# Optimization experiments

Hardware: AMD Instinct MI355X
Metric: run time of the kernel (lower is better)

The kernel has to match this reference:

```python
import jax, jax.numpy as jnp
import numpy as np


def setup_inputs() -> dict:
    key = jax.random.key(0)
    k1, k2 = jax.random.split(key)
    B, N, M, D = 16, 2048, 2048, 3
    predictions = jax.random.normal(k1, (B, N, D), dtype=jnp.float32)
    targets = jax.random.normal(k2, (B, M, D), dtype=jnp.float32)
    return {"predictions": predictions, "targets": targets}


def reference(predictions, targets):
    # Batched pairwise squared distances: [B, N, M]
    # d(i,j) = |x_i|^2 + |y_j|^2 - 2 x_i . y_j
    xx = jnp.sum(predictions * predictions, axis=-1)  # [B, N]
    yy = jnp.sum(targets * targets, axis=-1)          # [B, M]
    xy = jnp.einsum("bnd,bmd->bnm", predictions, targets)  # [B, N, M]
    P = xx[:, :, None] + yy[:, None, :] - 2.0 * xy    # [B, N, M]
    # Chamfer: sum of per-point nearest-neighbor squared distances, both directions
    loss = jnp.sum(jnp.min(P, axis=2)) + jnp.sum(jnp.min(P, axis=1))
    return loss
```

## Files before the change

### kernel.cpp

```cpp
#include <hip/hip_runtime.h>
#include <math.h>


typedef float v2f __attribute__((ext_vector_type(2)));

#define NPTS    2048
#define NCOMBO  32
#define KSLICE  32
#define SLICE   64
#define SPT     16
#define NBLK2   256

__device__ __forceinline__ v2f pkfma(v2f a, v2f b, v2f c) {
#if __has_builtin(__builtin_elementwise_fma)
    return __builtin_elementwise_fma(a, b, c);
#else
    v2f d; d.x = fmaf(a.x, b.x, c.x); d.y = fmaf(a.y, b.y, c.y); return d;
#endif
}

__global__ __launch_bounds__(256, 2) void chamfer_partial(
    const float* __restrict__ preds,
    const float* __restrict__ tgts,
    float* __restrict__ partial,
    int* __restrict__ counter)
{
    __shared__ __align__(16) float qx[2][SLICE];
    __shared__ __align__(16) float qy[2][SLICE];
    __shared__ __align__(16) float qz[2][SLICE];
    __shared__ __align__(16) float qw[2][SLICE];

    const int bid   = blockIdx.x;
    const int combo = bid & (NCOMBO - 1);
    const int spair = bid >> 5;
    const int dir   = combo >> 4;
    const int b     = combo & 15;

    const int sb    = threadIdx.x >> 7;
    const int tt    = threadIdx.x & 127;
    const int slice = spair * 2 + sb;

    if (bid == 0 && threadIdx.x == 0) *counter = 0;

    const float* src = (dir ? tgts : preds) + (size_t)b * NPTS * 3;
    const float* opp = (dir ? preds : tgts) + (size_t)b * NPTS * 3;

    if (tt < SLICE) {
        const int jj = slice * SLICE + tt;
        const float y0 = opp[3 * jj + 0];
        const float y1 = opp[3 * jj + 1];
        const float y2 = opp[3 * jj + 2];
        qx[sb][tt] = y0;
        qy[sb][tt] = y1;
        qz[sb][tt] = y2;
        qw[sb][tt] = y0 * y0 + y1 * y1 + y2 * y2;
    }

    v2f nn0[SPT], nn1[SPT], nn2[SPT];
    float m[SPT];
    #pragma unroll
    for (int k = 0; k < SPT; k++) {
        const int i = tt + 128 * k;
        const float a0 = -2.0f * src[3 * i + 0];
        const float a1 = -2.0f * src[3 * i + 1];
        const float a2 = -2.0f * src[3 * i + 2];
        nn0[k] = (v2f){a0, a0};
        nn1[k] = (v2f){a1, a1};
        nn2[k] = (v2f){a2, a2};
        m[k]   = INFINITY;
    }
    __syncthreads();

    #pragma unroll 2
    for (int jg = 0; jg < SLICE / 4; jg++) {
        const float4 X = *(const float4*)&qx[sb][4 * jg];
        const float4 Y = *(const float4*)&qy[sb][4 * jg];
        const float4 Z = *(const float4*)&qz[sb][4 * jg];
        const float4 W = *(const float4*)&qw[sb][4 * jg];
        const v2f Xa = {X.x, X.y}, Xb = {X.z, X.w};
        const v2f Ya = {Y.x, Y.y}, Yb = {Y.z, Y.w};
        const v2f Za = {Z.x, Z.y}, Zb = {Z.z, Z.w};
        const v2f Wa = {W.x, W.y}, Wb = {W.z, W.w};
        #pragma unroll
        for (int k = 0; k < SPT; k++) {
            const v2f sa = pkfma(nn0[k], Xa, pkfma(nn1[k], Ya, pkfma(nn2[k], Za, Wa)));
            m[k] = fminf(fminf(m[k], sa.x), sa.y);
            const v2f sb2 = pkfma(nn0[k], Xb, pkfma(nn1[k], Yb, pkfma(nn2[k], Zb, Wb)));
            m[k] = fminf(fminf(m[k], sb2.x), sb2.y);
        }
    }

    float* pp = partial + ((size_t)combo * KSLICE + slice) * NPTS;
    #pragma unroll
    for (int k = 0; k < SPT; k++)
        pp[tt + 128 * k] = m[k];
}

__global__ __launch_bounds__(256) void chamfer_reduce(
    const float* __restrict__ preds,
    const float* __restrict__ tgts,
    const float* __restrict__ partial,
    float* __restrict__ blocksum,
    int* __restrict__ counter,
    float* __restrict__ out)
{
    __shared__ float wsum[4];
    __shared__ bool  amLast;

    const int idx   = blockIdx.x * 256 + threadIdx.x;
    const int combo = idx >> 11;
    const int i     = idx & (NPTS - 1);
    const int dir   = combo >> 4;
    const int b     = combo & 15;

    const float* src = (dir ? tgts : preds) + (size_t)b * NPTS * 3;
    const float x0 = src[3 * i + 0];
    const float x1 = src[3 * i + 1];
    const float x2 = src[3 * i + 2];
    const float xx = x0 * x0 + x1 * x1 + x2 * x2;

    const float* pp = partial + (size_t)combo * KSLICE * NPTS + i;
    float mn = pp[0];
    #pragma unroll
    for (int s = 1; s < KSLICE; s++)
        mn = fminf(mn, pp[(size_t)s * NPTS]);

    float val = xx + mn;

    #pragma unroll
    for (int off = 32; off > 0; off >>= 1)
        val += __shfl_down(val, off, 64);

    const int lane = threadIdx.x & 63;
    const int wid  = threadIdx.x >> 6;
    if (lane == 0) wsum[wid] = val;
    __syncthreads();

    if (threadIdx.x == 0) {
        const float bsum = wsum[0] + wsum[1] + wsum[2] + wsum[3];
        __hip_atomic_store(&blocksum[blockIdx.x], bsum,
                           __ATOMIC_RELAXED, __HIP_MEMORY_SCOPE_AGENT);
        __threadfence();
        amLast = (atomicAdd(counter, 1) == NBLK2 - 1);
    }
    __syncthreads();

    if (amLast) {
        __threadfence();
        float v = __hip_atomic_load(&blocksum[threadIdx.x],
                                    __ATOMIC_RELAXED, __HIP_MEMORY_SCOPE_AGENT);
        #pragma unroll
        for (int off = 32; off > 0; off >>= 1)
            v += __shfl_down(v, off, 64);
        if (lane == 0) wsum[wid] = v;
        __syncthreads();
        if (threadIdx.x == 0)
            out[0] = wsum[0] + wsum[1] + wsum[2] + wsum[3];
    }
}

extern "C" void kernel_launch(void* const* d_in, const int* in_sizes, int n_in,
                              void* d_out, int out_size, void* d_ws, size_t ws_size,
                              hipStream_t stream) {
    const float* preds = (const float*)d_in[0];
    const float* tgts  = (const float*)d_in[1];
    float* out      = (float*)d_out;
    float* partial  = (float*)d_ws;
    float* blocksum = partial + (size_t)NCOMBO * KSLICE * NPTS;
    int*   counter  = (int*)(blocksum + NBLK2);

    chamfer_partial<<<NCOMBO * (KSLICE / 2), 256, 0, stream>>>(preds, tgts, partial, counter);
    chamfer_reduce<<<NBLK2, 256, 0, stream>>>(preds, tgts, partial, blocksum, counter, out);
}
```

Before: 77.06 us.

## Fuse partial-min and reduction kernels via per-combo last-block atomics

Merges the two kernels into one. The last block to finish each (direction, batch) combo, detected with a per-combo atomic counter, reduces that combo's 32 slice minima using float4 loads and adds the squared norms. A global counter then picks the final block to sum the 32 combo sums. This removes the second kernel launch and its gap, but adds a memset launch and serializes each combo's reduction into a single block.

Result: slower. 102.1 us (+32.5%).

```diff
diff --git a/kernel.cpp b/kernel.cpp
--- a/kernel.cpp
+++ b/kernel.cpp
@@ -9,7 +9,6 @@
 #define KSLICE  32
 #define SLICE   64
 #define SPT     16
-#define NBLK2   256
 
 __device__ __forceinline__ v2f pkfma(v2f a, v2f b, v2f c) {
 #if __has_builtin(__builtin_elementwise_fma)
@@ -19,16 +18,26 @@
 #endif
 }
 
-__global__ __launch_bounds__(256, 2) void chamfer_partial(
+__device__ __forceinline__ float4 fmin4(float4 a, float4 b) {
+    return make_float4(fminf(a.x, b.x), fminf(a.y, b.y),
+                       fminf(a.z, b.z), fminf(a.w, b.w));
+}
+
+__global__ __launch_bounds__(256, 2) void chamfer_fused(
     const float* __restrict__ preds,
     const float* __restrict__ tgts,
     float* __restrict__ partial,
-    int* __restrict__ counter)
+    float* __restrict__ combosum,
+    int* __restrict__ ccount,
+    int* __restrict__ gcount,
+    float* __restrict__ out)
 {
     __shared__ __align__(16) float qx[2][SLICE];
     __shared__ __align__(16) float qy[2][SLICE];
     __shared__ __align__(16) float qz[2][SLICE];
     __shared__ __align__(16) float qw[2][SLICE];
+    __shared__ float wsum[4];
+    __shared__ bool  amLast, amLast2;
 
     const int bid   = blockIdx.x;
     const int combo = bid & (NCOMBO - 1);
@@ -39,8 +48,6 @@
     const int sb    = threadIdx.x >> 7;
     const int tt    = threadIdx.x & 127;
     const int slice = spair * 2 + sb;
-
-    if (bid == 0 && threadIdx.x == 0) *counter = 0;
 
     const float* src = (dir ? tgts : preds) + (size_t)b * NPTS * 3;
     const float* opp = (dir ? preds : tgts) + (size_t)b * NPTS * 3;
@@ -94,43 +101,46 @@
     #pragma unroll
     for (int k = 0; k < SPT; k++)
         pp[tt + 128 * k] = m[k];
-}
 
-__global__ __launch_bounds__(256) void chamfer_reduce(
-    const float* __restrict__ preds,
-    const float* __restrict__ tgts,
-    const float* __restrict__ partial,
-    float* __restrict__ blocksum,
-    int* __restrict__ counter,
-    float* __restrict__ out)
-{
-    __shared__ float wsum[4];
-    __shared__ bool  amLast;
+    __syncthreads();
+    if (threadIdx.x == 0) {
+        __threadfence();
+        const int old = __hip_atomic_fetch_add(&ccount[combo], 1,
+                            __ATOMIC_ACQ_REL, __HIP_MEMORY_SCOPE_AGENT);
+        amLast = (old == 15);
+    }
+    __syncthreads();
+    if (!amLast) return;
+    __threadfence();
 
-    const int idx   = blockIdx.x * 256 + threadIdx.x;
-    const int combo = idx >> 11;
-    const int i     = idx & (NPTS - 1);
-    const int dir   = combo >> 4;
-    const int b     = combo & 15;
-
-    const float* src = (dir ? tgts : preds) + (size_t)b * NPTS * 3;
-    const float x0 = src[3 * i + 0];
-    const float x1 = src[3 * i + 1];
-    const float x2 = src[3 * i + 2];
-    const float xx = x0 * x0 + x1 * x1 + x2 * x2;
-
-    const float* pp = partial + (size_t)combo * KSLICE * NPTS + i;
-    float mn = pp[0];
-    #pragma unroll
-    for (int s = 1; s < KSLICE; s++)
-        mn = fminf(mn, pp[(size_t)s * NPTS]);
-
-    float val = xx + mn;
+    const float* base = partial + (size_t)combo * KSLICE * NPTS;
+    const int t = threadIdx.x;
+    float4 mnA = make_float4(INFINITY, INFINITY, INFINITY, INFINITY);
+    float4 mnB = mnA;
+    #pragma unroll 4
+    for (int s = 0; s < KSLICE; s++) {
+        mnA = fmin4(mnA, *(const float4*)&base[(size_t)s * NPTS + 4 * t]);
+        mnB = fmin4(mnB, *(const float4*)&base[(size_t)s * NPTS + 1024 + 4 * t]);
+    }
+    const float4 rA0 = *(const float4*)&src[12 * t + 0];
+    const float4 rA1 = *(const float4*)&src[12 * t + 4];
+    const float4 rA2 = *(const float4*)&src[12 * t + 8];
+    const float4 rB0 = *(const float4*)&src[3072 + 12 * t + 0];
+    const float4 rB1 = *(const float4*)&src[3072 + 12 * t + 4];
+    const float4 rB2 = *(const float4*)&src[3072 + 12 * t + 8];
+    float val =
+        (fmaf(rA0.x, rA0.x, fmaf(rA0.y, rA0.y, rA0.z * rA0.z)) + mnA.x) +
+        (fmaf(rA0.w, rA0.w, fmaf(rA1.x, rA1.x, rA1.y * rA1.y)) + mnA.y) +
+        (fmaf(rA1.z, rA1.z, fmaf(rA1.w, rA1.w, rA2.x * rA2.x)) + mnA.z) +
+        (fmaf(rA2.y, rA2.y, fmaf(rA2.z, rA2.z, rA2.w * rA2.w)) + mnA.w) +
+        (fmaf(rB0.x, rB0.x, fmaf(rB0.y, rB0.y, rB0.z * rB0.z)) + mnB.x) +
+        (fmaf(rB0.w, rB0.w, fmaf(rB1.x, rB1.x, rB1.y * rB1.y)) + mnB.y) +
+        (fmaf(rB1.z, rB1.z, fmaf(rB1.w, rB1.w, rB2.x * rB2.x)) + mnB.z) +
+        (fmaf(rB2.y, rB2.y, fmaf(rB2.z, rB2.z, rB2.w * rB2.w)) + mnB.w);
 
     #pragma unroll
     for (int off = 32; off > 0; off >>= 1)
         val += __shfl_down(val, off, 64);
-
     const int lane = threadIdx.x & 63;
     const int wid  = threadIdx.x >> 6;
     if (lane == 0) wsum[wid] = val;
@@ -138,24 +148,26 @@
 
     if (threadIdx.x == 0) {
         const float bsum = wsum[0] + wsum[1] + wsum[2] + wsum[3];
-        __hip_atomic_store(&blocksum[blockIdx.x], bsum,
+        __hip_atomic_store(&combosum[combo], bsum,
                            __ATOMIC_RELAXED, __HIP_MEMORY_SCOPE_AGENT);
         __threadfence();
-        amLast = (atomicAdd(counter, 1) == NBLK2 - 1);
+        const int old = __hip_atomic_fetch_add(gcount, 1,
+                            __ATOMIC_ACQ_REL, __HIP_MEMORY_SCOPE_AGENT);
+        amLast2 = (old == NCOMBO - 1);
     }
     __syncthreads();
+    if (!amLast2) return;
+    __threadfence();
 
-    if (amLast) {
-        __threadfence();
-        float v = __hip_atomic_load(&blocksum[threadIdx.x],
-                                    __ATOMIC_RELAXED, __HIP_MEMORY_SCOPE_AGENT);
+    if (threadIdx.x < 64) {
+        float v = (threadIdx.x < NCOMBO)
+            ? __hip_atomic_load(&combosum[threadIdx.x],
+                                __ATOMIC_RELAXED, __HIP_MEMORY_SCOPE_AGENT)
+            : 0.0f;
         #pragma unroll
         for (int off = 32; off > 0; off >>= 1)
             v += __shfl_down(v, off, 64);
-        if (lane == 0) wsum[wid] = v;
-        __syncthreads();
-        if (threadIdx.x == 0)
-            out[0] = wsum[0] + wsum[1] + wsum[2] + wsum[3];
+        if (threadIdx.x == 0) out[0] = v;
     }
 }
 
@@ -166,9 +178,11 @@
     const float* tgts  = (const float*)d_in[1];
     float* out      = (float*)d_out;
     float* partial  = (float*)d_ws;
-    float* blocksum = partial + (size_t)NCOMBO * KSLICE * NPTS;
-    int*   counter  = (int*)(blocksum + NBLK2);
+    float* combosum = partial + (size_t)NCOMBO * KSLICE * NPTS;
+    int*   ccount   = (int*)(combosum + NCOMBO);
+    int*   gcount   = ccount + NCOMBO;
 
-    chamfer_partial<<<NCOMBO * (KSLICE / 2), 256, 0, stream>>>(preds, tgts, partial, counter);
-    chamfer_reduce<<<NBLK2, 256, 0, stream>>>(preds, tgts, partial, blocksum, counter, out);
+    hipMemsetAsync(ccount, 0, (NCOMBO + 1) * sizeof(int), stream);
+    chamfer_fused<<<NCOMBO * (KSLICE / 2), 256, 0, stream>>>(
+        preds, tgts, partial, combosum, ccount, gcount, out);
 }
```
